# Kernel optimization log

Measured on AMD Instinct MI355X. Metric: run time of the kernel, lower is better.

The kernel has to match this reference:

```python
import jax, jax.numpy as jnp
import numpy as np

ROI = 268          # nodes per graph / input feature dim
G = 512            # graphs in batch
N = G * ROI        # total nodes = 137216
E = 1000000        # total edges
CH = 32            # GIN hidden channels
SLOPE = 0.33       # leaky relu negative slope
BN_EPS = 1e-5


def _leaky(h):
    return jnp.where(h > 0, h, SLOPE * h)


def _bn(h, g, b, m, v):
    # inference-mode batch norm with running stats
    return (h - m) * jax.lax.rsqrt(v + BN_EPS) * g + b


def _gin(x, src, dst, eps, W1, b1, W2, b2, g, b, m, v):
    # GINConv: mlp((1+eps)*x + sum_{j->i} x_j), then BN + LeakyReLU
    agg = jax.ops.segment_sum(x[src], dst, num_segments=x.shape[0])
    h = (1.0 + eps) * x + agg
    h = _leaky(h @ W1 + b1) @ W2 + b2
    return _leaky(_bn(h, g, b, m, v))


def _pool(x, batch, counts):
    mx = jax.ops.segment_max(x, batch, num_segments=G)
    mn = jax.ops.segment_sum(x, batch, num_segments=G) / counts[:, None]
    return jnp.concatenate([mx, mn], axis=-1)


def setup_inputs() -> dict:
    key = jax.random.key(0)
    ks = jax.random.split(key, 16)
    x = jax.random.normal(ks[0], (N, ROI), dtype=jnp.float32)
    # edges constrained within each graph: node = graph_id*ROI + local_idx
    gid = jax.random.randint(ks[1], (E,), 0, G, dtype=jnp.int32)
    src = gid * ROI + jax.random.randint(ks[2], (E,), 0, ROI, dtype=jnp.int32)
    dst = gid * ROI + jax.random.randint(ks[3], (E,), 0, ROI, dtype=jnp.int32)
    edge_index = jnp.stack([src, dst], axis=0)
    batch = jnp.repeat(jnp.arange(G, dtype=jnp.int32), ROI)

    def lin(k, fi, fo):
        return jax.random.normal(k, (fi, fo), dtype=jnp.float32) / np.sqrt(fi)

    kp = jax.random.split(ks[4], 16)
    inp = {
        'x': x, 'edge_index': edge_index, 'batch': batch,
        # GIN layer 0 (268 -> 32)
        'eps0': jnp.zeros((), jnp.float32),
        'W1_0': lin(kp[0], ROI, CH), 'b1_0': jnp.zeros((CH,), jnp.float32),
        'W2_0': lin(kp[1], CH, CH), 'b2_0': jnp.zeros((CH,), jnp.float32),
        'bn0_g': jnp.ones((CH,), jnp.float32), 'bn0_b': jnp.zeros((CH,), jnp.float32),
        'bn0_m': jnp.zeros((CH,), jnp.float32), 'bn0_v': jnp.ones((CH,), jnp.float32),
        # GIN layer 1 (32 -> 32)
        'eps1': jnp.zeros((), jnp.float32),
        'W1_1': lin(kp[2], CH, CH), 'b1_1': jnp.zeros((CH,), jnp.float32),
        'W2_1': lin(kp[3], CH, CH), 'b2_1': jnp.zeros((CH,), jnp.float32),
        'bn1_g': jnp.ones((CH,), jnp.float32), 'bn1_b': jnp.zeros((CH,), jnp.float32),
        'bn1_m': jnp.zeros((CH,), jnp.float32), 'bn1_v': jnp.ones((CH,), jnp.float32),
        # readout head: 4*CH=128 -> 256 -> 128 -> 1
        'lin1_W': lin(kp[4], 4 * CH, 256), 'lin1_b': jnp.zeros((256,), jnp.float32),
        'hbn1_g': jnp.ones((256,), jnp.float32), 'hbn1_b': jnp.zeros((256,), jnp.float32),
        'hbn1_m': jnp.zeros((256,), jnp.float32), 'hbn1_v': jnp.ones((256,), jnp.float32),
        'lin2_W': lin(kp[5], 256, 128), 'lin2_b': jnp.zeros((128,), jnp.float32),
        'hbn2_g': jnp.ones((128,), jnp.float32), 'hbn2_b': jnp.zeros((128,), jnp.float32),
        'hbn2_m': jnp.zeros((128,), jnp.float32), 'hbn2_v': jnp.ones((128,), jnp.float32),
        'lin3_W': lin(kp[6], 128, 1), 'lin3_b': jnp.zeros((1,), jnp.float32),
    }
    return inp


def reference(x, edge_index, batch,
              eps0, W1_0, b1_0, W2_0, b2_0, bn0_g, bn0_b, bn0_m, bn0_v,
              eps1, W1_1, b1_1, W2_1, b2_1, bn1_g, bn1_b, bn1_m, bn1_v,
              lin1_W, lin1_b, hbn1_g, hbn1_b, hbn1_m, hbn1_v,
              lin2_W, lin2_b, hbn2_g, hbn2_b, hbn2_m, hbn2_v,
              lin3_W, lin3_b):
    src, dst = edge_index[0], edge_index[1]
    counts = jax.ops.segment_sum(jnp.ones((x.shape[0],), x.dtype), batch, num_segments=G)
    h0 = _gin(x, src, dst, eps0, W1_0, b1_0, W2_0, b2_0, bn0_g, bn0_b, bn0_m, bn0_v)
    p0 = _pool(h0, batch, counts)                      # [G, 2*CH]
    h1 = _gin(h0, src, dst, eps1, W1_1, b1_1, W2_1, b2_1, bn1_g, bn1_b, bn1_m, bn1_v)
    p1 = _pool(h1, batch, counts)                      # [G, 2*CH]
    z = jnp.concatenate([p0, p1], axis=-1)             # [G, 4*CH]
    z = _leaky(_bn(z @ lin1_W + lin1_b, hbn1_g, hbn1_b, hbn1_m, hbn1_v))
    z = _leaky(_bn(z @ lin2_W + lin2_b, hbn2_g, hbn2_b, hbn2_m, hbn2_v))
    return z @ lin3_W + lin3_b                          # [G, 1]
```

## Files before the change

### kernel.cpp

```cpp
#include <hip/hip_runtime.h>

#define ROI 268
#define NG 512
#define NNODES (NG * ROI)
#define CH 32
#define SLOPE 0.33f
#define BN_EPS 1e-5f
#define SR 33
#define SAS 258
#define RPS (ROI + 1)
#define CAP 2560
#define NB_G1 (NNODES / 256)
#define NB_BKT 128

typedef unsigned short u16;
typedef unsigned int u32;

__device__ __forceinline__ float leakyf(float v) {
    return v > 0.f ? v : SLOPE * v;
}

__global__ __launch_bounds__(256)
__attribute__((amdgpu_waves_per_eu(4, 4))) void k_gemmbkt(
    const float* __restrict__ x, const float* __restrict__ W1,
    float* __restrict__ y0, const int* __restrict__ src,
    const int* __restrict__ dst, int E, int* __restrict__ gcnt,
    u32* __restrict__ pairs) {
    __shared__ float sW[32 * CH];
    __shared__ float sA[32 * SAS];

    const int tid = threadIdx.x;

    if (blockIdx.x >= NB_G1) {
        int* hist = (int*)sW;
        int* gb = (int*)sW + 512;
        for (int i = tid; i < 512; i += 256) hist[i] = 0;
        __syncthreads();
        const int b = blockIdx.x - NB_G1;
        const int chunk = (E + NB_BKT - 1) / NB_BKT;
        const int i0 = b * chunk;
        const int i1 = (i0 + chunk < E) ? (i0 + chunk) : E;
        for (int i = i0 + tid; i < i1; i += 256) {
            int g = dst[i] / ROI;
            atomicAdd(&hist[g], 1);
        }
        __syncthreads();
        for (int g = tid; g < 512; g += 256) {
            int h = hist[g];
            gb[g] = h ? atomicAdd(&gcnt[g], h) : 0;
            hist[g] = 0;
        }
        __syncthreads();
        for (int i = i0 + tid; i < i1; i += 256) {
            int d = dst[i];
            int g = d / ROI;
            int loc = atomicAdd(&hist[g], 1);
            int pos = gb[g] + loc;
            if (pos < CAP)
                pairs[(size_t)g * CAP + pos] =
                    ((u32)(d - g * ROI) << 16) | (u32)((src[i] - g * ROI) * SR);
        }
        return;
    }

    const int l = tid & 63;
    const int wcb = __builtin_amdgcn_readfirstlane((tid >> 6) << 3);
    const size_t rowbase = (size_t)blockIdx.x * 256;

    float acc[4][8];
#pragma unroll
    for (int r = 0; r < 4; r++)
#pragma unroll
        for (int c = 0; c < 8; c++) acc[r][c] = 0.f;

    float4 pf[8];
#pragma unroll
    for (int i = 0; i < 8; i++) {
        int f = (i << 8) + tid;
        int row = f >> 3, kc = (f & 7) << 2;
        pf[i] = *(const float4*)&x[(rowbase + row) * ROI + kc];
    }
    float4 pw = ((const float4*)W1)[tid];

    int k0 = 0;
    for (int chunk = 0; chunk < 9; ++chunk) {
        const int ksize = (chunk < 8) ? 32 : 12;
        if (ksize == 32) {
#pragma unroll
            for (int i = 0; i < 8; i++) {
                int f = (i << 8) + tid;
                int row = f >> 3, kc = (f & 7) << 2;
                sA[(kc + 0) * SAS + row] = pf[i].x;
                sA[(kc + 1) * SAS + row] = pf[i].y;
                sA[(kc + 2) * SAS + row] = pf[i].z;
                sA[(kc + 3) * SAS + row] = pf[i].w;
            }
            ((float4*)sW)[tid] = pw;
        } else {
#pragma unroll
            for (int i = 0; i < 3; i++) {
                int kc = i << 2;
                sA[(kc + 0) * SAS + tid] = pf[i].x;
                sA[(kc + 1) * SAS + tid] = pf[i].y;
                sA[(kc + 2) * SAS + tid] = pf[i].z;
                sA[(kc + 3) * SAS + tid] = pf[i].w;
            }
            if (tid < 96) ((float4*)sW)[tid] = pw;
        }
        __syncthreads();
        if (chunk + 1 < 9) {
            const int nk0 = k0 + ksize;
            if (chunk + 1 < 8) {
#pragma unroll
                for (int i = 0; i < 8; i++) {
                    int f = (i << 8) + tid;
                    int row = f >> 3, kc = (f & 7) << 2;
                    pf[i] = *(const float4*)&x[(rowbase + row) * ROI + nk0 + kc];
                }
                pw = ((const float4*)(W1 + nk0 * CH))[tid];
            } else {
#pragma unroll
                for (int i = 0; i < 3; i++)
                    pf[i] = *(const float4*)&x[(rowbase + tid) * ROI + nk0 + (i << 2)];
                if (tid < 96) pw = ((const float4*)(W1 + nk0 * CH))[tid];
            }
        }
        const float* wp = &sW[wcb];
#pragma unroll 2
        for (int kk = 0; kk < ksize; ++kk) {
            float2 a0 = *(const float2*)&sA[kk * SAS + 2 * l];
            float2 a1 = *(const float2*)&sA[kk * SAS + 128 + 2 * l];
            float4 w0 = *(const float4*)&wp[kk * CH];
            float4 w1 = *(const float4*)&wp[kk * CH + 4];
            float av[4] = {a0.x, a0.y, a1.x, a1.y};
            float wv[8] = {w0.x, w0.y, w0.z, w0.w, w1.x, w1.y, w1.z, w1.w};
#pragma unroll
            for (int r = 0; r < 4; r++)
#pragma unroll
                for (int c = 0; c < 8; c++) acc[r][c] += av[r] * wv[c];
        }
        k0 += ksize;
        __syncthreads();
    }

#pragma unroll
    for (int r = 0; r < 4; r++) {
        size_t row = rowbase + ((r < 2) ? (2 * l + r) : (126 + 2 * l + r));
        *(float4*)&y0[row * CH + wcb] =
            make_float4(acc[r][0], acc[r][1], acc[r][2], acc[r][3]);
        *(float4*)&y0[row * CH + wcb + 4] =
            make_float4(acc[r][4], acc[r][5], acc[r][6], acc[r][7]);
    }
}

__device__ __forceinline__ void gather_combine(
    const float* __restrict__ in, float* __restrict__ out,
    const int* __restrict__ rpl, const u16* __restrict__ ebg, float e,
    const float* __restrict__ b1, int t) {
    const int ch = t & 31;
    const int hw = t >> 5;
    for (int n = hw; n < ROI; n += 16) {
        int b = rpl[n], en = rpl[n + 1];
        float acc = 0.f;
        int j = b;
        for (; j + 3 < en; j += 4) {
            int p0 = ebg[j], p1 = ebg[j + 1], p2 = ebg[j + 2], p3 = ebg[j + 3];
            float v0 = in[p0 + ch], v1 = in[p1 + ch];
            float v2 = in[p2 + ch], v3 = in[p3 + ch];
            acc += (v0 + v1) + (v2 + v3);
        }
        for (; j < en; ++j) acc += in[ebg[j] + ch];
        out[n * SR + ch] = leakyf(e * in[n * SR + ch] + acc + b1[ch]);
    }
}

template <bool AFFINE>
__device__ __forceinline__ void gemm_inplace(float* __restrict__ buf,
                                             const float* __restrict__ w,
                                             const float* __restrict__ bias,
                                             const float* __restrict__ sc,
                                             const float* __restrict__ sh, int t) {
    for (int u = t; u < ROI * 2; u += 512) {
        const int r0 = (u >> 2) * 2;
        const int cq = u & 3;
        float acc0[8], acc1[8];
#pragma unroll
        for (int c = 0; c < 8; c++) {
            float b = AFFINE ? bias[cq * 8 + c] : 0.f;
            acc0[c] = b;
            acc1[c] = b;
        }
        const float* row0 = &buf[r0 * SR];
        const float* row1 = row0 + SR;
#pragma unroll 2
        for (int k = 0; k < CH; k += 2) {
            float2 a0 = *(const float2*)&row0[k];
            float2 a1 = *(const float2*)&row1[k];
            const float* wr0 = &w[k * CH + cq * 8];
            const float* wr1 = wr0 + CH;
            float4 wa = *(const float4*)wr0;
            float4 wb = *(const float4*)(wr0 + 4);
            float4 wc = *(const float4*)wr1;
            float4 wd = *(const float4*)(wr1 + 4);
            acc0[0] += a0.x * wa.x + a0.y * wc.x;
            acc0[1] += a0.x * wa.y + a0.y * wc.y;
            acc0[2] += a0.x * wa.z + a0.y * wc.z;
            acc0[3] += a0.x * wa.w + a0.y * wc.w;
            acc0[4] += a0.x * wb.x + a0.y * wd.x;
            acc0[5] += a0.x * wb.y + a0.y * wd.y;
            acc0[6] += a0.x * wb.z + a0.y * wd.z;
            acc0[7] += a0.x * wb.w + a0.y * wd.w;
            acc1[0] += a1.x * wa.x + a1.y * wc.x;
            acc1[1] += a1.x * wa.y + a1.y * wc.y;
            acc1[2] += a1.x * wa.z + a1.y * wc.z;
            acc1[3] += a1.x * wa.w + a1.y * wc.w;
            acc1[4] += a1.x * wb.x + a1.y * wd.x;
            acc1[5] += a1.x * wb.y + a1.y * wd.y;
            acc1[6] += a1.x * wb.z + a1.y * wd.z;
            acc1[7] += a1.x * wb.w + a1.y * wd.w;
        }
        float* o0 = &buf[r0 * SR + cq * 8];
        float* o1 = o0 + SR;
#pragma unroll
        for (int c = 0; c < 8; c += 2) {
            float h00 = acc0[c], h01 = acc0[c + 1];
            float h10 = acc1[c], h11 = acc1[c + 1];
            if (AFFINE) {
                float s0 = sc[cq * 8 + c], t0 = sh[cq * 8 + c];
                float s1 = sc[cq * 8 + c + 1], t1 = sh[cq * 8 + c + 1];
                h00 = leakyf(h00 * s0 + t0);
                h01 = leakyf(h01 * s1 + t1);
                h10 = leakyf(h10 * s0 + t0);
                h11 = leakyf(h11 * s1 + t1);
            }
            *(float2*)&o0[c] = make_float2(h00, h01);
            *(float2*)&o1[c] = make_float2(h10, h11);
        }
    }
}

__device__ __forceinline__ void pool_store(const float* __restrict__ h,
                                           float* __restrict__ psc, int t) {
    const int ch = t & 31;
    const int hw = t >> 5;
    const int wave = t >> 6;
    float s = 0.f, m = -1e30f;
    for (int n = hw; n < ROI; n += 16) {
        float v = h[n * SR + ch];
        s += v;
        m = fmaxf(m, v);
    }
    s += __shfl_down(s, 32);
    m = fmaxf(m, __shfl_down(m, 32));
    if ((t & 63) < 32) {
        psc[wave * 32 + ch] = s;
        psc[256 + wave * 32 + ch] = m;
    }
}

__device__ __forceinline__ void pool_final(const float* __restrict__ psc,
                                           float* __restrict__ zg, int t) {
    if (t < 32) {
        float s = 0.f, m = -1e30f;
#pragma unroll
        for (int wv = 0; wv < 8; wv++) {
            s += psc[wv * 32 + t];
            m = fmaxf(m, psc[256 + wv * 32 + t]);
        }
        zg[t] = m;
        zg[CH + t] = s / (float)ROI;
    }
}

__global__ __launch_bounds__(512, 2) void k_gin(
    const float* __restrict__ y0, const int* __restrict__ gcnt,
    const u32* __restrict__ pairs, u16* __restrict__ ebuf,
    const float* __restrict__ eps0p,
    const float* __restrict__ b1_0, const float* __restrict__ W2_0,
    const float* __restrict__ b2_0, const float* __restrict__ bn0_g,
    const float* __restrict__ bn0_b, const float* __restrict__ bn0_m,
    const float* __restrict__ bn0_v, const float* __restrict__ eps1p,
    const float* __restrict__ W1_1, const float* __restrict__ b1_1,
    const float* __restrict__ W2_1, const float* __restrict__ b2_1,
    const float* __restrict__ bn1_g, const float* __restrict__ bn1_b,
    const float* __restrict__ bn1_m, const float* __restrict__ bn1_v,
    float* __restrict__ z) {
    __shared__ float bufA[ROI * SR];
    __shared__ float bufB[ROI * SR];
    __shared__ float w[CH * CH];
    __shared__ int rpl[RPS];
    __shared__ float prm[8 * CH];
    __shared__ float psc[512];
    __shared__ float epss[2];

    const int t = threadIdx.x;
    const int g = blockIdx.x;
    const u32* pg = pairs + (size_t)g * CAP;
    u16* ebg = ebuf + (size_t)g * CAP;
    const int cnt = (gcnt[g] < CAP) ? gcnt[g] : CAP;

    if (t < CH) {
        prm[0 * CH + t] = b1_0[t];
        prm[1 * CH + t] = b2_0[t];
        float s0 = bn0_g[t] * rsqrtf(bn0_v[t] + BN_EPS);
        prm[2 * CH + t] = s0;
        prm[3 * CH + t] = bn0_b[t] - bn0_m[t] * s0;
        prm[4 * CH + t] = b1_1[t];
        prm[5 * CH + t] = b2_1[t];
        float s1 = bn1_g[t] * rsqrtf(bn1_v[t] + BN_EPS);
        prm[6 * CH + t] = s1;
        prm[7 * CH + t] = bn1_b[t] - bn1_m[t] * s1;
    }
    if (t == 0) {
        epss[0] = 1.0f + *eps0p;
        epss[1] = 1.0f + *eps1p;
    }
    if (t < RPS) rpl[t] = 0;

    const float* yg = y0 + (size_t)g * ROI * CH;
    for (int f = t; f < (ROI * CH) / 4; f += 512) {
        float4 v = ((const float4*)yg)[f];
        int row = f >> 3, c4 = (f & 7) << 2;
        float* p = &bufA[row * SR + c4];
        *(float2*)p = make_float2(v.x, v.y);
        *(float2*)(p + 2) = make_float2(v.z, v.w);
    }
    for (int i = t; i < (CH * CH) / 4; i += 512)
        ((float4*)w)[i] = ((const float4*)W2_0)[i];
    __syncthreads();

    for (int i = t; i < cnt; i += 512) atomicAdd(&rpl[pg[i] >> 16], 1);
    __syncthreads();
    int* s = (int*)psc;
    int v = (t < ROI) ? rpl[t] : 0;
    s[t] = v;
    __syncthreads();
    for (int d = 1; d < 512; d <<= 1) {
        int u = (t >= d) ? s[t - d] : 0;
        __syncthreads();
        s[t] += u;
        __syncthreads();
    }
    int inc = s[t];
    if (t < ROI) rpl[t] = inc - v;
    if (t == 511) rpl[ROI] = inc;
    __syncthreads();
    int* cur = (int*)psc;
    if (t < ROI) cur[t] = rpl[t];
    __syncthreads();
    for (int i = t; i < cnt; i += 512) {
        u32 p = pg[i];
        int pos = atomicAdd(&cur[p >> 16], 1);
        ebg[pos] = (u16)(p & 0xffffu);
    }
    __syncthreads();

    gather_combine(bufA, bufB, rpl, ebg, epss[0], &prm[0 * CH], t);
    __syncthreads();

    gemm_inplace<true>(bufB, w, &prm[1 * CH], &prm[2 * CH], &prm[3 * CH], t);
    __syncthreads();

    pool_store(bufB, psc, t);
    for (int i = t; i < (CH * CH) / 4; i += 512)
        ((float4*)w)[i] = ((const float4*)W1_1)[i];
    __syncthreads();

    pool_final(psc, z + (size_t)g * 128, t);
    gemm_inplace<false>(bufB, w, nullptr, nullptr, nullptr, t);
    __syncthreads();

    gather_combine(bufB, bufA, rpl, ebg, epss[1], &prm[4 * CH], t);
    for (int i = t; i < (CH * CH) / 4; i += 512)
        ((float4*)w)[i] = ((const float4*)W2_1)[i];
    __syncthreads();

    gemm_inplace<true>(bufA, w, &prm[5 * CH], &prm[6 * CH], &prm[7 * CH], t);
    __syncthreads();

    pool_store(bufA, psc, t);
    __syncthreads();
    pool_final(psc, z + (size_t)g * 128 + 64, t);
}

__global__ __launch_bounds__(256) void k_head(
    const float* __restrict__ z, const float* __restrict__ W1,
    const float* __restrict__ b1, const float* __restrict__ g1,
    const float* __restrict__ be1, const float* __restrict__ m1,
    const float* __restrict__ v1, const float* __restrict__ W2,
    const float* __restrict__ b2, const float* __restrict__ g2,
    const float* __restrict__ be2, const float* __restrict__ m2,
    const float* __restrict__ v2, const float* __restrict__ W3,
    const float* __restrict__ b3, float* __restrict__ out) {
    __shared__ float zr[128], z1[256], z2[128];
    const int t = threadIdx.x;
    const int g = blockIdx.x;

    if (t < 32) ((float4*)zr)[t] = ((const float4*)(z + (size_t)g * 128))[t];
    __syncthreads();
    {
        float acc = b1[t];
#pragma unroll 8
        for (int k = 0; k < 128; k++) acc += zr[k] * W1[k * 256 + t];
        float s = g1[t] * rsqrtf(v1[t] + BN_EPS);
        acc = (acc - m1[t]) * s + be1[t];
        z1[t] = leakyf(acc);
    }
    __syncthreads();
    if (t < 128) {
        float acc = b2[t];
#pragma unroll 8
        for (int k = 0; k < 256; k++) acc += z1[k] * W2[k * 128 + t];
        float s = g2[t] * rsqrtf(v2[t] + BN_EPS);
        acc = (acc - m2[t]) * s + be2[t];
        z2[t] = leakyf(acc);
    }
    __syncthreads();
    if (t < 64) {
        float v = z2[t] * W3[t] + z2[t + 64] * W3[t + 64];
        for (int offd = 32; offd; offd >>= 1) v += __shfl_down(v, offd);
        if (t == 0) out[g] = v + b3[0];
    }
}

extern "C" void kernel_launch(void* const* d_in, const int* in_sizes, int n_in,
                              void* d_out, int out_size, void* d_ws, size_t ws_size,
                              hipStream_t stream) {
    const float* x      = (const float*)d_in[0];
    const int* eidx     = (const int*)d_in[1];
    const float* eps0   = (const float*)d_in[3];
    const float* W1_0   = (const float*)d_in[4];
    const float* b1_0   = (const float*)d_in[5];
    const float* W2_0   = (const float*)d_in[6];
    const float* b2_0   = (const float*)d_in[7];
    const float* bn0_g  = (const float*)d_in[8];
    const float* bn0_b  = (const float*)d_in[9];
    const float* bn0_m  = (const float*)d_in[10];
    const float* bn0_v  = (const float*)d_in[11];
    const float* eps1   = (const float*)d_in[12];
    const float* W1_1   = (const float*)d_in[13];
    const float* b1_1   = (const float*)d_in[14];
    const float* W2_1   = (const float*)d_in[15];
    const float* b2_1   = (const float*)d_in[16];
    const float* bn1_g  = (const float*)d_in[17];
    const float* bn1_b  = (const float*)d_in[18];
    const float* bn1_m  = (const float*)d_in[19];
    const float* bn1_v  = (const float*)d_in[20];
    const float* lin1_W = (const float*)d_in[21];
    const float* lin1_b = (const float*)d_in[22];
    const float* hbn1_g = (const float*)d_in[23];
    const float* hbn1_b = (const float*)d_in[24];
    const float* hbn1_m = (const float*)d_in[25];
    const float* hbn1_v = (const float*)d_in[26];
    const float* lin2_W = (const float*)d_in[27];
    const float* lin2_b = (const float*)d_in[28];
    const float* hbn2_g = (const float*)d_in[29];
    const float* hbn2_b = (const float*)d_in[30];
    const float* hbn2_m = (const float*)d_in[31];
    const float* hbn2_v = (const float*)d_in[32];
    const float* lin3_W = (const float*)d_in[33];
    const float* lin3_b = (const float*)d_in[34];

    const int E = in_sizes[1] / 2;
    const int* src = eidx;
    const int* dst = eidx + E;

    char* ws = (char*)d_ws;
    const size_t Y0_OFF = 0;
    const size_t Z_OFF  = (size_t)NNODES * CH * 4;
    const size_t GC_OFF = Z_OFF + (size_t)NG * 128 * 4;
    const size_t PR_OFF = GC_OFF + 2048;
    const size_t EB_OFF = PR_OFF + (size_t)NG * CAP * 4;

    float* y0  = (float*)(ws + Y0_OFF);
    float* z   = (float*)(ws + Z_OFF);
    int* gcnt  = (int*)(ws + GC_OFF);
    u32* pairs = (u32*)(ws + PR_OFF);
    u16* ebuf  = (u16*)(ws + EB_OFF);

    hipMemsetAsync(gcnt, 0, 2048, stream);
    k_gemmbkt<<<NB_G1 + NB_BKT, 256, 0, stream>>>(x, W1_0, y0, src, dst, E,
                                                  gcnt, pairs);

    k_gin<<<NG, 512, 0, stream>>>(y0, gcnt, pairs, ebuf, eps0, b1_0, W2_0,
                                  b2_0, bn0_g, bn0_b, bn0_m, bn0_v, eps1,
                                  W1_1, b1_1, W2_1, b2_1, bn1_g, bn1_b,
                                  bn1_m, bn1_v, z);

    k_head<<<NG, 256, 0, stream>>>(z, lin1_W, lin1_b, hbn1_g, hbn1_b, hbn1_m,
                                   hbn1_v, lin2_W, lin2_b, hbn2_g, hbn2_b,
                                   hbn2_m, hbn2_v, lin3_W, lin3_b,
                                   (float*)d_out);
}
```

Measured before the change: 422.1 us.

## Halve GEMM row tile and fuse MLP head into GIN kernel

The first GEMM kernel now processes 128 rows per block instead of 256, with half the accumulators and a smaller LDS tile, and its waves-per-EU hint is relaxed to allow higher occupancy. Separately, the head MLP (lin1/lin2/lin3 with BN and LeakyReLU) is moved into the end of the per-graph GIN kernel. This removes one kernel launch and the round trip of pooled features through global memory. The trade-off is more blocks and less per-thread reuse in the GEMM, and extra per-block tail work inside the GIN kernel.

```diff
diff --git a/kernel.cpp b/kernel.cpp
--- a/kernel.cpp
+++ b/kernel.cpp
@@ -7,10 +7,10 @@
 #define SLOPE 0.33f
 #define BN_EPS 1e-5f
 #define SR 33
-#define SAS 258
+#define SAS2 130
 #define RPS (ROI + 1)
 #define CAP 2560
-#define NB_G1 (NNODES / 256)
+#define NB_G1 (NNODES / 128)
 #define NB_BKT 128
 
 typedef unsigned short u16;
@@ -21,13 +21,13 @@
 }
 
 __global__ __launch_bounds__(256)
-__attribute__((amdgpu_waves_per_eu(4, 4))) void k_gemmbkt(
+__attribute__((amdgpu_waves_per_eu(4, 8))) void k_gemmbkt(
     const float* __restrict__ x, const float* __restrict__ W1,
     float* __restrict__ y0, const int* __restrict__ src,
     const int* __restrict__ dst, int E, int* __restrict__ gcnt,
     u32* __restrict__ pairs) {
     __shared__ float sW[32 * CH];
-    __shared__ float sA[32 * SAS];
+    __shared__ float sA[32 * SAS2];
 
     const int tid = threadIdx.x;
 
@@ -65,17 +65,17 @@
 
     const int l = tid & 63;
     const int wcb = __builtin_amdgcn_readfirstlane((tid >> 6) << 3);
-    const size_t rowbase = (size_t)blockIdx.x * 256;
-
-    float acc[4][8];
-#pragma unroll
-    for (int r = 0; r < 4; r++)
+    const size_t rowbase = (size_t)blockIdx.x * 128;
+
+    float acc[2][8];
+#pragma unroll
+    for (int r = 0; r < 2; r++)
 #pragma unroll
         for (int c = 0; c < 8; c++) acc[r][c] = 0.f;
 
-    float4 pf[8];
-#pragma unroll
-    for (int i = 0; i < 8; i++) {
+    float4 pf[4];
+#pragma unroll
+    for (int i = 0; i < 4; i++) {
         int f = (i << 8) + tid;
         int row = f >> 3, kc = (f & 7) << 2;
         pf[i] = *(const float4*)&x[(rowbase + row) * ROI + kc];
@@ -87,23 +87,25 @@
         const int ksize = (chunk < 8) ? 32 : 12;
         if (ksize == 32) {
 #pragma unroll
-            for (int i = 0; i < 8; i++) {
+            for (int i = 0; i < 4; i++) {
                 int f = (i << 8) + tid;
                 int row = f >> 3, kc = (f & 7) << 2;
-                sA[(kc + 0) * SAS + row] = pf[i].x;
-                sA[(kc + 1) * SAS + row] = pf[i].y;
-                sA[(kc + 2) * SAS + row] = pf[i].z;
-                sA[(kc + 3) * SAS + row] = pf[i].w;
+                sA[(kc + 0) * SAS2 + row] = pf[i].x;
+                sA[(kc + 1) * SAS2 + row] = pf[i].y;
+                sA[(kc + 2) * SAS2 + row] = pf[i].z;
+                sA[(kc + 3) * SAS2 + row] = pf[i].w;
             }
             ((float4*)sW)[tid] = pw;
         } else {
-#pragma unroll
-            for (int i = 0; i < 3; i++) {
-                int kc = i << 2;
-                sA[(kc + 0) * SAS + tid] = pf[i].x;
-                sA[(kc + 1) * SAS + tid] = pf[i].y;
-                sA[(kc + 2) * SAS + tid] = pf[i].z;
-                sA[(kc + 3) * SAS + tid] = pf[i].w;
+            if (tid < 128) {
+#pragma unroll
+                for (int i = 0; i < 3; i++) {
+                    int kc = i << 2;
+                    sA[(kc + 0) * SAS2 + tid] = pf[i].x;
+                    sA[(kc + 1) * SAS2 + tid] = pf[i].y;
+                    sA[(kc + 2) * SAS2 + tid] = pf[i].z;
+                    sA[(kc + 3) * SAS2 + tid] = pf[i].w;
+                }
             }
             if (tid < 96) ((float4*)sW)[tid] = pw;
         }
@@ -112,40 +114,40 @@
             const int nk0 = k0 + ksize;
             if (chunk + 1 < 8) {
 #pragma unroll
-                for (int i = 0; i < 8; i++) {
+                for (int i = 0; i < 4; i++) {
                     int f = (i << 8) + tid;
                     int row = f >> 3, kc = (f & 7) << 2;
                     pf[i] = *(const float4*)&x[(rowbase + row) * ROI + nk0 + kc];
                 }
                 pw = ((const float4*)(W1 + nk0 * CH))[tid];
             } else {
-#pragma unroll
-                for (int i = 0; i < 3; i++)
-                    pf[i] = *(const float4*)&x[(rowbase + tid) * ROI + nk0 + (i << 2)];
+                if (tid < 128) {
+#pragma unroll
+                    for (int i = 0; i < 3; i++)
+                        pf[i] = *(const float4*)&x[(rowbase + tid) * ROI + nk0 + (i << 2)];
+                }
                 if (tid < 96) pw = ((const float4*)(W1 + nk0 * CH))[tid];
             }
         }
         const float* wp = &sW[wcb];
 #pragma unroll 2
         for (int kk = 0; kk < ksize; ++kk) {
-            float2 a0 = *(const float2*)&sA[kk * SAS + 2 * l];
-            float2 a1 = *(const float2*)&sA[kk * SAS + 128 + 2 * l];
+            float2 a0 = *(const float2*)&sA[kk * SAS2 + 2 * l];
             float4 w0 = *(const float4*)&wp[kk * CH];
             float4 w1 = *(const float4*)&wp[kk * CH + 4];
-            float av[4] = {a0.x, a0.y, a1.x, a1.y};
             float wv[8] = {w0.x, w0.y, w0.z, w0.w, w1.x, w1.y, w1.z, w1.w};
 #pragma unroll
-            for (int r = 0; r < 4; r++)
-#pragma unroll
-                for (int c = 0; c < 8; c++) acc[r][c] += av[r] * wv[c];
+            for (int c = 0; c < 8; c++) acc[0][c] += a0.x * wv[c];
+#pragma unroll
+            for (int c = 0; c < 8; c++) acc[1][c] += a0.y * wv[c];
         }
         k0 += ksize;
         __syncthreads();
     }
 
 #pragma unroll
-    for (int r = 0; r < 4; r++) {
-        size_t row = rowbase + ((r < 2) ? (2 * l + r) : (126 + 2 * l + r));
+    for (int r = 0; r < 2; r++) {
+        size_t row = rowbase + 2 * l + r;
         *(float4*)&y0[row * CH + wcb] =
             make_float4(acc[r][0], acc[r][1], acc[r][2], acc[r][3]);
         *(float4*)&y0[row * CH + wcb + 4] =
@@ -284,13 +286,21 @@
     const float* __restrict__ W2_1, const float* __restrict__ b2_1,
     const float* __restrict__ bn1_g, const float* __restrict__ bn1_b,
     const float* __restrict__ bn1_m, const float* __restrict__ bn1_v,
-    float* __restrict__ z) {
+    const float* __restrict__ hW1, const float* __restrict__ hb1,
+    const float* __restrict__ hg1, const float* __restrict__ hbe1,
+    const float* __restrict__ hm1, const float* __restrict__ hv1,
+    const float* __restrict__ hW2, const float* __restrict__ hb2,
+    const float* __restrict__ hg2, const float* __restrict__ hbe2,
+    const float* __restrict__ hm2, const float* __restrict__ hv2,
+    const float* __restrict__ hW3, const float* __restrict__ hb3,
+    float* __restrict__ out) {
     __shared__ float bufA[ROI * SR];
     __shared__ float bufB[ROI * SR];
     __shared__ float w[CH * CH];
     __shared__ int rpl[RPS];
     __shared__ float prm[8 * CH];
     __shared__ float psc[512];
+    __shared__ float zloc[128];
     __shared__ float epss[2];
 
     const int t = threadIdx.x;
@@ -366,7 +376,7 @@
         ((float4*)w)[i] = ((const float4*)W1_1)[i];
     __syncthreads();
 
-    pool_final(psc, z + (size_t)g * 128, t);
+    pool_final(psc, zloc, t);
     gemm_inplace<false>(bufB, w, nullptr, nullptr, nullptr, t);
     __syncthreads();
 
@@ -380,46 +390,32 @@
 
     pool_store(bufA, psc, t);
     __syncthreads();
-    pool_final(psc, z + (size_t)g * 128 + 64, t);
-}
-
-__global__ __launch_bounds__(256) void k_head(
-    const float* __restrict__ z, const float* __restrict__ W1,
-    const float* __restrict__ b1, const float* __restrict__ g1,
-    const float* __restrict__ be1, const float* __restrict__ m1,
-    const float* __restrict__ v1, const float* __restrict__ W2,
-    const float* __restrict__ b2, const float* __restrict__ g2,
-    const float* __restrict__ be2, const float* __restrict__ m2,
-    const float* __restrict__ v2, const float* __restrict__ W3,
-    const float* __restrict__ b3, float* __restrict__ out) {
-    __shared__ float zr[128], z1[256], z2[128];
-    const int t = threadIdx.x;
-    const int g = blockIdx.x;
-
-    if (t < 32) ((float4*)zr)[t] = ((const float4*)(z + (size_t)g * 128))[t];
-    __syncthreads();
-    {
-        float acc = b1[t];
+    pool_final(psc, zloc + 64, t);
+    __syncthreads();
+
+    float* h1 = psc;
+    if (t < 256) {
+        float a = hb1[t];
 #pragma unroll 8
-        for (int k = 0; k < 128; k++) acc += zr[k] * W1[k * 256 + t];
-        float s = g1[t] * rsqrtf(v1[t] + BN_EPS);
-        acc = (acc - m1[t]) * s + be1[t];
-        z1[t] = leakyf(acc);
+        for (int k = 0; k < 128; k++) a += zloc[k] * hW1[k * 256 + t];
+        float sc = hg1[t] * rsqrtf(hv1[t] + BN_EPS);
+        a = (a - hm1[t]) * sc + hbe1[t];
+        h1[t] = leakyf(a);
     }
     __syncthreads();
     if (t < 128) {
-        float acc = b2[t];
+        float a = hb2[t];
 #pragma unroll 8
-        for (int k = 0; k < 256; k++) acc += z1[k] * W2[k * 128 + t];
-        float s = g2[t] * rsqrtf(v2[t] + BN_EPS);
-        acc = (acc - m2[t]) * s + be2[t];
-        z2[t] = leakyf(acc);
+        for (int k = 0; k < 256; k++) a += h1[k] * hW2[k * 128 + t];
+        float sc = hg2[t] * rsqrtf(hv2[t] + BN_EPS);
+        a = (a - hm2[t]) * sc + hbe2[t];
+        zloc[t] = leakyf(a);
     }
     __syncthreads();
     if (t < 64) {
-        float v = z2[t] * W3[t] + z2[t + 64] * W3[t + 64];
-        for (int offd = 32; offd; offd >>= 1) v += __shfl_down(v, offd);
-        if (t == 0) out[g] = v + b3[0];
+        float vv = zloc[t] * hW3[t] + zloc[t + 64] * hW3[t + 64];
+        for (int offd = 32; offd; offd >>= 1) vv += __shfl_down(vv, offd);
+        if (t == 0) out[g] = vv + hb3[0];
     }
 }
 
@@ -467,13 +463,11 @@
 
     char* ws = (char*)d_ws;
     const size_t Y0_OFF = 0;
-    const size_t Z_OFF  = (size_t)NNODES * CH * 4;
-    const size_t GC_OFF = Z_OFF + (size_t)NG * 128 * 4;
+    const size_t GC_OFF = (size_t)NNODES * CH * 4;
     const size_t PR_OFF = GC_OFF + 2048;
     const size_t EB_OFF = PR_OFF + (size_t)NG * CAP * 4;
 
     float* y0  = (float*)(ws + Y0_OFF);
-    float* z   = (float*)(ws + Z_OFF);
     int* gcnt  = (int*)(ws + GC_OFF);
     u32* pairs = (u32*)(ws + PR_OFF);
     u16* ebuf  = (u16*)(ws + EB_OFF);
@@ -485,10 +479,9 @@
     k_gin<<<NG, 512, 0, stream>>>(y0, gcnt, pairs, ebuf, eps0, b1_0, W2_0,
                                   b2_0, bn0_g, bn0_b, bn0_m, bn0_v, eps1,
                                   W1_1, b1_1, W2_1, b2_1, bn1_g, bn1_b,
-                                  bn1_m, bn1_v, z);
-
-    k_head<<<NG, 256, 0, stream>>>(z, lin1_W, lin1_b, hbn1_g, hbn1_b, hbn1_m,
-                                   hbn1_v, lin2_W, lin2_b, hbn2_g, hbn2_b,
-                                   hbn2_m, hbn2_v, lin3_W, lin3_b,
-                                   (float*)d_out);
-}
+                                  bn1_m, bn1_v,
+                                  lin1_W, lin1_b, hbn1_g, hbn1_b, hbn1_m,
+                                  hbn1_v, lin2_W, lin2_b, hbn2_g, hbn2_b,
+                                  hbn2_m, hbn2_v, lin3_W, lin3_b,
+                                  (float*)d_out);
+}
```

After: 412.5 us. 1.02x faster.
